# Kernel tuning notes

Measured on AMD Instinct MI355X. Metric: run time of the kernel, lower is better.

## Reference

```python
import jax, jax.numpy as jnp
import numpy as np

N = 32768   # nodes
E = 32768   # edges
ND, ED, GD = 12, 5, 11
H = 64
T = 4
STEPS = 3


def setup_inputs() -> dict:
    key = jax.random.key(0)
    ks = jax.random.split(key, 24)
    s = 0.05
    p = lambda k, sh: (jax.random.normal(k, sh) * s).astype(jnp.float32)
    return dict(
        x=jax.random.normal(ks[0], (N, ND), jnp.float32),
        edge_index=jax.random.randint(ks[1], (2, E), 0, N, jnp.int64),
        edge_attr=jax.random.uniform(ks[2], (E, ED), jnp.float32),
        u=jax.random.normal(ks[3], (1, GD), jnp.float32),
        Wp=p(ks[4], (H, ND + GD)), bp=p(ks[5], (H,)),
        We1=p(ks[6], (H, ED)), be1=p(ks[7], (H,)),
        We2=p(ks[8], (H * H, H)), be2=p(ks[9], (H * H,)),
        root=p(ks[10], (H, H)), conv_b=p(ks[11], (H,)),
        Wih=p(ks[12], (3 * H, H)), bih=p(ks[13], (3 * H,)),
        Whh=p(ks[14], (3 * H, H)), bhh=p(ks[15], (3 * H,)),
        Wd1=p(ks[16], (H, 2 * H + ED)), bd1=p(ks[17], (H,)),
        Wd2=p(ks[18], (H // 2, H)), bd2=p(ks[19], (H // 2,)),
        Wd3=p(ks[20], (T, H // 2)), bd3=p(ks[21], (T,)),
    )


def _forward(x, edge_index, edge_attr, u,
             Wp, bp, We1, be1, We2, be2, root, conv_b,
             Wih, bih, Whh, bhh, Wd1, bd1, Wd2, bd2, Wd3, bd3):
    n = x.shape[0]
    e = edge_attr.shape[0]
    src, dst = edge_index[0], edge_index[1]

    # input projection with broadcast global features (batch=None path)
    u_node = jnp.broadcast_to(u, (n, u.shape[-1]))
    h = jnp.tanh(jnp.concatenate([x, u_node], axis=-1) @ Wp.T + bp)

    # edge MLP -> per-edge (H,H) weight matrices; edge_attr is loop-invariant
    ew = jax.nn.relu(edge_attr @ We1.T + be1) @ We2.T + be2   # (E, H*H)
    ew = ew.reshape(e, H, H)                                   # (E, H, H)

    # mean-aggregation denominators (clamped to 1 like scatter-mean)
    counts = jnp.clip(jax.ops.segment_sum(jnp.ones((e,), h.dtype), dst, num_segments=n), 1.0)

    for _ in range(STEPS):
        # NNConv: gather src features, per-edge matmul, scatter-mean into dst
        msg = jnp.einsum('eh,eho->eo', h[src], ew)             # (E, H)
        agg = jax.ops.segment_sum(msg, dst, num_segments=n) / counts[:, None]
        m = jax.nn.relu(agg + h @ root + conv_b)               # dropout off (eval)
        # GRUCell (torch gate order: r, z, n)
        gi = m @ Wih.T + bih
        gh = h @ Whh.T + bhh
        r = jax.nn.sigmoid(gi[:, :H] + gh[:, :H])
        z = jax.nn.sigmoid(gi[:, H:2 * H] + gh[:, H:2 * H])
        ng = jnp.tanh(gi[:, 2 * H:] + r * gh[:, 2 * H:])
        h = (1.0 - z) * ng + z * h

    # per-edge decoder
    e_in = jnp.concatenate([h[src], h[dst], edge_attr], axis=-1)
    d = jax.nn.relu(e_in @ Wd1.T + bd1)
    d = jax.nn.relu(d @ Wd2.T + bd2)
    return d @ Wd3.T + bd3                                     # (E, T)


def reference(x, edge_index, edge_attr, u,
              Wp, bp, We1, be1, We2, be2, root, conv_b,
              Wih, bih, Whh, bhh, Wd1, bd1, Wd2, bd2, Wd3, bd3):
    return _forward(x, edge_index, edge_attr, u,
                    Wp, bp, We1, be1, We2, be2, root, conv_b,
                    Wih, bih, Whh, bhh, Wd1, bd1, Wd2, bd2, Wd3, bd3)
```

## Files before the change

### kernel.cpp

```cpp
#include <hip/hip_runtime.h>
#include <hip/hip_bf16.h>
#include <stdint.h>


#define N_NODES 32768
#define N_EDGES 32768
#define STEPS 3

typedef __attribute__((ext_vector_type(8))) short short8;
typedef __attribute__((ext_vector_type(4))) float float4v;

__device__ __forceinline__ float bf2f(unsigned short u) {
    union { unsigned int i; float f; } v; v.i = ((unsigned int)u) << 16; return v.f;
}
__device__ __forceinline__ unsigned short f2bf(float f) {
    union { float f; unsigned int i; } v; v.f = f;
    unsigned int x = v.i;
    return (unsigned short)((x + 0x7fffu + ((x >> 16) & 1u)) >> 16);
}
__device__ __forceinline__ unsigned int fbits(float f) {
    union { float f; unsigned int i; } v; v.f = f; return v.i;
}

__device__ __forceinline__ short8 packA(float hv, const float* hf) {
    union { short8 v; unsigned int u[4]; } r;
#pragma unroll
    for (int p = 0; p < 4; p++) {
        unsigned int p0 = fbits(hv * hf[2 * p]) + 0x8000u;
        unsigned int p1 = fbits(hv * hf[2 * p + 1]) + 0x8000u;
        r.u[p] = __builtin_amdgcn_perm(p1, p0, 0x07060302u);
    }
    return r.v;
}

__device__ __forceinline__ void gload_lds16(const void* g, void* l) {
    __builtin_amdgcn_global_load_lds(
        (__attribute__((address_space(1))) void*)g,
        (__attribute__((address_space(3))) void*)l, 16, 0, 0);
}

__global__ __launch_bounds__(256) void k_setup(
    const float* __restrict__ root, const float* __restrict__ Wih,
    const float* __restrict__ Whh,
    const float* __restrict__ We2, const float* __restrict__ be2,
    const float* __restrict__ Wd1, const float* __restrict__ bd1,
    const float* __restrict__ Wd2,
    const float* __restrict__ x, const float* __restrict__ u,
    const float* __restrict__ Wp, const float* __restrict__ bp,
    const float* __restrict__ ea, const float* __restrict__ We1,
    const float* __restrict__ be1,
    unsigned short* __restrict__ rootTf, unsigned short* __restrict__ wcombf,
    unsigned short* __restrict__ w2tf,
    unsigned short* __restrict__ wd1f, unsigned short* __restrict__ wd2f,
    unsigned short* __restrict__ hb,
    unsigned short* __restrict__ hid, float* __restrict__ aggcnt)
{
    int b = blockIdx.x, tid = threadIdx.x;
    if (b < 144) {
        int i = b * 256 + tid;
        if (i < 4096) {
            int j = i & 7, lane = (i >> 3) & 63, g = i >> 9;
            int kb = g >> 2, nf = g & 3;
            int o = nf * 16 + (lane & 15);
            int k = kb * 32 + (lane >> 4) * 8 + j;
            rootTf[i] = f2bf(root[k * 64 + o]);
        } else if (i < 4096 + 32768) {
            int t = i - 4096;
            int j = t & 7, lane = (t >> 3) & 63, g = t >> 9;
            int kb = g >> 4, nf = g & 15;
            int cp = nf * 16 + (lane & 15);
            int k = kb * 32 + (lane >> 4) * 8 + j;
            float v;
            if (cp < 128)      v = (k < 64) ? Wih[cp * 64 + k] : Whh[cp * 64 + (k - 64)];
            else if (cp < 192) v = (k < 64) ? Wih[cp * 64 + k] : 0.f;
            else               v = (k < 64) ? 0.f : Whh[(cp - 64) * 64 + (k - 64)];
            wcombf[t] = f2bf(v);
        }
    } else if (b < 1184) {
        int t = (b - 144) * 256 + tid;
        if (t < 65 * 4096) {
            int kk = t >> 12, r = t & 4095;
            int j = r & 7, lane = (r >> 3) & 63, g = r >> 9;
            int half = g >> 2, nf = g & 3;
            int o = nf * 16 + (lane & 15);
            int hh = half * 32 + (lane >> 4) * 8 + j;
            float v = (kk < 64) ? We2[((size_t)(hh * 64 + o)) * 64 + kk]
                                : be2[(size_t)hh * 64 + o];
            w2tf[t] = f2bf(v);
        }
    } else if (b < 1232) {
        int i = (b - 1184) * 256 + tid;
        if (i < 10240) {
            int j = i & 7, lane = (i >> 3) & 63, g = i >> 9;
            int kb = g >> 2, nf = g & 3;
            int o = nf * 16 + (lane & 15);
            int k = kb * 32 + (lane >> 4) * 8 + j;
            float v = (k < 133) ? Wd1[(size_t)o * 133 + k] : (k == 133 ? bd1[o] : 0.f);
            wd1f[i] = f2bf(v);
        } else if (i < 10240 + 2048) {
            int t = i - 10240;
            int j = t & 7, lane = (t >> 3) & 63, g = t >> 9;
            int kb = g >> 1, nf = g & 1;
            int o = nf * 16 + (lane & 15);
            int k = kb * 32 + (lane >> 4) * 8 + j;
            wd2f[t] = f2bf(Wd2[(size_t)o * 64 + k]);
        }
    } else if (b < 9424) {
        int idx = (b - 1232) * 256 + tid;
        int n = idx >> 6, j = idx & 63;
        const float* wr = Wp + j * 23;
        const float* xr = x + (size_t)n * 12;
        float s = bp[j];
#pragma unroll
        for (int i = 0; i < 12; i++) s += xr[i] * wr[i];
#pragma unroll
        for (int i = 0; i < 11; i++) s += u[i] * wr[12 + i];
        hb[idx] = f2bf(tanhf(s));
    } else if (b < 17616) {
        int idx = (b - 9424) * 256 + tid;
        int e = idx >> 6, j = idx & 63;
        float s = be1[j];
#pragma unroll
        for (int i = 0; i < 5; i++) s += ea[(size_t)e * 5 + i] * We1[j * 5 + i];
        hid[idx] = f2bf(s > 0.f ? s : 0.f);
    } else {
        int idx = (b - 17616) * 1024 + tid * 4;
        if (idx < 2129920) {
            float4v z = {0.f, 0.f, 0.f, 0.f};
            *(float4v*)(aggcnt + idx) = z;
        }
    }
}

__global__ __launch_bounds__(256) void k_counts(
    const int* __restrict__ ei, float* __restrict__ counts)
{
    int i = blockIdx.x * 256 + threadIdx.x;
    if (i < N_EDGES) atomicAdd(&counts[ei[N_EDGES + i]], 1.0f);
}

__global__ __launch_bounds__(512, 4) void k_msg_fused(
    const unsigned short* __restrict__ hid,
    const unsigned short* __restrict__ hb,
    const unsigned short* __restrict__ w2tf,
    const int* __restrict__ ei,
    float* __restrict__ agg)
{
    __shared__ unsigned short buf[2][2][8192];
    int tid = threadIdx.x, wave = tid >> 6, lane = tid & 63;
    int l15 = lane & 15, quad = lane >> 4;
    int mf = wave & 3, kh = wave >> 2;
    int ebase = blockIdx.x * 64 + mf * 16;
    int e_a = ebase + l15;
    int src = ei[e_a];

    union { short8 v[4]; unsigned short u[32]; } hrow;
#pragma unroll
    for (int i = 0; i < 4; i++)
        hrow.v[i] = *(const short8*)(hid + (size_t)e_a * 64 + kh * 32 + i * 8);

    float hf0[8], hf1[8];
    {
        short8 h0 = *(const short8*)(hb + (size_t)src * 64 + quad * 8);
        short8 h1 = *(const short8*)(hb + (size_t)src * 64 + 32 + quad * 8);
#pragma unroll
        for (int j = 0; j < 8; j++) {
            hf0[j] = bf2f((unsigned short)h0[j]);
            hf1[j] = bf2f((unsigned short)h1[j]);
        }
    }

    int kk0 = kh ? 32 : 0;
    auto stage = [&](int pair, int db) {
        const unsigned short* g = w2tf + (size_t)(kk0 + 2 * pair) * 4096;
#pragma unroll
        for (int c = 0; c < 4; c++) {
            int chunk = mf * 4 + c;
            gload_lds16(g + (size_t)chunk * 512 + lane * 8, &buf[kh][db][chunk * 512]);
        }
    };

    stage(0, 0);

    float4v acc[4] = {};
    int cur = 0;
#pragma unroll
    for (int i = 0; i <= 16; i++) {
        __syncthreads();
        if ((kh == 0 && i + 1 < 16) || (kh == 1 && i + 1 <= 16))
            stage(i + 1, cur ^ 1);
        int nkk = (kh == 0) ? (i < 16 ? 2 : 0) : (i < 16 ? 2 : 1);
        for (int s = 0; s < nkk; s++) {
            float hv = (kh == 1 && i == 16) ? 1.0f : bf2f(hrow.u[2 * i + s]);
            short8 a0 = packA(hv, hf0);
            short8 a1 = packA(hv, hf1);
            const unsigned short* bp = &buf[kh][cur][s * 4096];
#pragma unroll
            for (int nf = 0; nf < 4; nf++) {
                short8 b0 = *(const short8*)(bp + (0 * 4 + nf) * 512 + lane * 8);
                acc[nf] = __builtin_amdgcn_mfma_f32_16x16x32_bf16(a0, b0, acc[nf], 0, 0, 0);
            }
#pragma unroll
            for (int nf = 0; nf < 4; nf++) {
                short8 b1 = *(const short8*)(bp + (1 * 4 + nf) * 512 + lane * 8);
                acc[nf] = __builtin_amdgcn_mfma_f32_16x16x32_bf16(a1, b1, acc[nf], 0, 0, 0);
            }
        }
        cur ^= 1;
    }

    __syncthreads();
    float* mg = (float*)&buf[0][0][0];
    if (kh == 1) {
#pragma unroll
        for (int nf = 0; nf < 4; nf++)
#pragma unroll
            for (int r = 0; r < 4; r++)
                mg[mf * 1024 + lane * 16 + nf * 4 + r] = acc[nf][r];
    }
    __syncthreads();
    if (kh == 0) {
        int dsts[4];
#pragma unroll
        for (int r = 0; r < 4; r++) dsts[r] = ei[N_EDGES + ebase + quad * 4 + r];
#pragma unroll
        for (int nf = 0; nf < 4; nf++)
#pragma unroll
            for (int r = 0; r < 4; r++)
                atomicAdd(agg + (size_t)dsts[r] * 64 + nf * 16 + l15,
                          acc[nf][r] + mg[mf * 1024 + lane * 16 + nf * 4 + r]);
    }
}

__global__ __launch_bounds__(256) void k_node(
    const unsigned short* __restrict__ hb_in,
    const unsigned short* __restrict__ rootTf,
    const unsigned short* __restrict__ wcombf,
    float* __restrict__ agg, const float* __restrict__ counts,
    const float* __restrict__ conv_b,
    const float* __restrict__ bih, const float* __restrict__ bhh,
    unsigned short* __restrict__ hb_out)
{
    __shared__ unsigned short m_lds[64 * 72];
    int tid = threadIdx.x, w = tid >> 6, lane = tid & 63;
    int l15 = lane & 15, quad = lane >> 4;
    int node0 = blockIdx.x * 64;
    int row0 = w * 16;

    float4v acc1[4] = {};
    {
        short8 a1[2];
#pragma unroll
        for (int kb = 0; kb < 2; kb++)
            a1[kb] = *(const short8*)(hb_in + (size_t)(node0 + row0 + l15) * 64 + kb * 32 + quad * 8);
#pragma unroll
        for (int kb = 0; kb < 2; kb++)
#pragma unroll
            for (int nf = 0; nf < 4; nf++) {
                short8 b = *(const short8*)(rootTf + (size_t)((kb * 4 + nf) * 64 + lane) * 8);
                acc1[nf] = __builtin_amdgcn_mfma_f32_16x16x32_bf16(a1[kb], b, acc1[nf], 0, 0, 0);
            }
    }
#pragma unroll
    for (int rr = 0; rr < 4; rr++) {
        int nl = row0 + quad * 4 + rr;
        float cnt = counts[node0 + nl]; if (cnt < 1.f) cnt = 1.f;
        float rcp = 1.f / cnt;
#pragma unroll
        for (int nf = 0; nf < 4; nf++) {
            int c = nf * 16 + l15;
            float* ap = agg + (size_t)(node0 + nl) * 64 + c;
            float av = *ap;
            *ap = 0.f;
            float mv = av * rcp + acc1[nf][rr] + conv_b[c];
            m_lds[nl * 72 + c] = f2bf(mv > 0.f ? mv : 0.f);
        }
    }
    __syncthreads();

    float4v acc2[16] = {};
#pragma unroll
    for (int kb = 0; kb < 4; kb++) {
        short8 a2;
        if (kb < 2)
            a2 = *(const short8*)(m_lds + (row0 + l15) * 72 + kb * 32 + quad * 8);
        else
            a2 = *(const short8*)(hb_in + (size_t)(node0 + row0 + l15) * 64 + (kb - 2) * 32 + quad * 8);
#pragma unroll
        for (int nf = 0; nf < 16; nf++) {
            short8 b = *(const short8*)(wcombf + (size_t)((kb * 16 + nf) * 64 + lane) * 8);
            acc2[nf] = __builtin_amdgcn_mfma_f32_16x16x32_bf16(a2, b, acc2[nf], 0, 0, 0);
        }
    }

#pragma unroll
    for (int nf0 = 0; nf0 < 4; nf0++) {
        int c = nf0 * 16 + l15;
        float br = bih[c] + bhh[c];
        float bz = bih[64 + c] + bhh[64 + c];
        float bni = bih[128 + c], bnh = bhh[128 + c];
#pragma unroll
        for (int rr = 0; rr < 4; rr++) {
            int node = node0 + row0 + quad * 4 + rr;
            float gr = 1.f / (1.f + __expf(-(acc2[nf0][rr] + br)));
            float gz = 1.f / (1.f + __expf(-(acc2[nf0 + 4][rr] + bz)));
            float ng = tanhf(acc2[nf0 + 8][rr] + bni + gr * (acc2[nf0 + 12][rr] + bnh));
            float ho = bf2f(hb_in[(size_t)node * 64 + c]);
            float hn = (1.f - gz) * ng + gz * ho;
            hb_out[(size_t)node * 64 + c] = f2bf(hn);
        }
    }
}

__global__ __launch_bounds__(256) void k_decoder(
    const unsigned short* __restrict__ hb, const int* __restrict__ ei,
    const float* __restrict__ ea,
    const unsigned short* __restrict__ wd1f, const unsigned short* __restrict__ wd2f,
    const float* __restrict__ bd2,
    const float* __restrict__ Wd3, const float* __restrict__ bd3,
    float* __restrict__ out)
{
    __shared__ unsigned short d1f[4][1024];
    __shared__ float d2s[4][16 * 33];
    int tid = threadIdx.x, w = tid >> 6, lane = tid & 63;
    int l15 = lane & 15, quad = lane >> 4;
    int ebase = blockIdx.x * 64 + w * 16;
    int e = ebase + l15;
    int src = ei[e], dst = ei[N_EDGES + e];

    short8 a[5];
#pragma unroll
    for (int kb = 0; kb < 2; kb++) {
        a[kb]     = *(const short8*)(hb + (size_t)src * 64 + kb * 32 + quad * 8);
        a[2 + kb] = *(const short8*)(hb + (size_t)dst * 64 + kb * 32 + quad * 8);
    }
    {
        union { short8 v; unsigned short u[8]; } tea;
#pragma unroll
        for (int j = 0; j < 8; j++) {
            float vv = 0.f;
            if (quad == 0) vv = (j < 5) ? ea[(size_t)e * 5 + j] : (j == 5 ? 1.f : 0.f);
            tea.u[j] = f2bf(vv);
        }
        a[4] = tea.v;
    }

    float4v acc1[4] = {};
#pragma unroll
    for (int kb = 0; kb < 5; kb++)
#pragma unroll
        for (int nf = 0; nf < 4; nf++) {
            short8 b = *(const short8*)(wd1f + (size_t)((kb * 4 + nf) * 64 + lane) * 8);
            acc1[nf] = __builtin_amdgcn_mfma_f32_16x16x32_bf16(a[kb], b, acc1[nf], 0, 0, 0);
        }
#pragma unroll
    for (int nf = 0; nf < 4; nf++) {
        int kbp = nf >> 1;
        int lanep_hi = ((nf & 1) * 2 + (l15 >> 3)) * 16;
        int jp = l15 & 7;
#pragma unroll
        for (int r = 0; r < 4; r++) {
            float v = acc1[nf][r];
            d1f[w][kbp * 512 + (lanep_hi + quad * 4 + r) * 8 + jp] = f2bf(v > 0.f ? v : 0.f);
        }
    }
    float4v acc2[2] = {};
#pragma unroll
    for (int kb = 0; kb < 2; kb++) {
        short8 a2 = *(const short8*)(&d1f[w][kb * 512 + lane * 8]);
#pragma unroll
        for (int nf = 0; nf < 2; nf++) {
            short8 b = *(const short8*)(wd2f + (size_t)((kb * 2 + nf) * 64 + lane) * 8);
            acc2[nf] = __builtin_amdgcn_mfma_f32_16x16x32_bf16(a2, b, acc2[nf], 0, 0, 0);
        }
    }
#pragma unroll
    for (int nf = 0; nf < 2; nf++) {
        int c = nf * 16 + l15;
        float bias = bd2[c];
#pragma unroll
        for (int r = 0; r < 4; r++) {
            float v = acc2[nf][r] + bias;
            d2s[w][(quad * 4 + r) * 33 + c] = v > 0.f ? v : 0.f;
        }
    }
    {
        int e_l = lane >> 2, t = lane & 3;
        float s = bd3[t];
        const float* w3 = Wd3 + t * 32;
        const float* dr = &d2s[w][e_l * 33];
#pragma unroll
        for (int k = 0; k < 32; k++) s += w3[k] * dr[k];
        out[(size_t)(ebase + e_l) * 4 + t] = s;
    }
}

extern "C" void kernel_launch(void* const* d_in, const int* in_sizes, int n_in,
                              void* d_out, int out_size, void* d_ws, size_t ws_size,
                              hipStream_t stream)
{
    const float* x      = (const float*)d_in[0];
    const int*   ei     = (const int*)d_in[1];
    const float* ea     = (const float*)d_in[2];
    const float* u      = (const float*)d_in[3];
    const float* Wp     = (const float*)d_in[4];
    const float* bp     = (const float*)d_in[5];
    const float* We1    = (const float*)d_in[6];
    const float* be1    = (const float*)d_in[7];
    const float* We2    = (const float*)d_in[8];
    const float* be2    = (const float*)d_in[9];
    const float* root   = (const float*)d_in[10];
    const float* conv_b = (const float*)d_in[11];
    const float* Wih    = (const float*)d_in[12];
    const float* bih    = (const float*)d_in[13];
    const float* Whh    = (const float*)d_in[14];
    const float* bhh    = (const float*)d_in[15];
    const float* Wd1    = (const float*)d_in[16];
    const float* bd1    = (const float*)d_in[17];
    const float* Wd2    = (const float*)d_in[18];
    const float* bd2    = (const float*)d_in[19];
    const float* Wd3    = (const float*)d_in[20];
    const float* bd3    = (const float*)d_in[21];
    float* out = (float*)d_out;

    char* ws = (char*)d_ws;
    size_t off = 0;
    auto take = [&](size_t bytes) -> char* {
        char* p = ws + off; off = (off + bytes + 255) & ~(size_t)255; return p;
    };
    unsigned short* hb     = (unsigned short*)take((size_t)N_NODES * 64 * 2);
    unsigned short* hid    = (unsigned short*)take((size_t)N_EDGES * 64 * 2);
    float*          aggcnt = (float*)take((size_t)(N_NODES * 64 + N_NODES) * 4);
    float*          agg    = aggcnt;
    float*          cnts   = aggcnt + (size_t)N_NODES * 64;
    unsigned short* w2tf   = (unsigned short*)take((size_t)66 * 4096 * 2);
    unsigned short* rootTf = (unsigned short*)take((size_t)4096 * 2);
    unsigned short* wcombf = (unsigned short*)take((size_t)32768 * 2);
    unsigned short* wd1f   = (unsigned short*)take((size_t)10240 * 2);
    unsigned short* wd2f   = (unsigned short*)take((size_t)2048 * 2);
    (void)ws_size;

    k_setup<<<19696, 256, 0, stream>>>(root, Wih, Whh, We2, be2, Wd1, bd1, Wd2,
                                       x, u, Wp, bp, ea, We1, be1,
                                       rootTf, wcombf, w2tf, wd1f, wd2f,
                                       hb, hid, aggcnt);
    k_counts<<<128, 256, 0, stream>>>(ei, cnts);

    for (int s = 0; s < STEPS; s++) {
        k_msg_fused<<<N_EDGES / 64, 512, 0, stream>>>(hid, hb, w2tf, ei, agg);
        k_node<<<N_NODES / 64, 256, 0, stream>>>(hb, rootTf, wcombf, agg, cnts,
                                                 conv_b, bih, bhh, hb);
    }
    k_decoder<<<N_EDGES / 64, 256, 0, stream>>>(hb, ei, ea, wd1f, wd2f, bd2,
                                                Wd3, bd3, out);
}
```

Before: 267.0 us.

## Switch bf16 storage and MFMA to fp16 with packed half2 products

Converts all stored activations and weights from bf16 to fp16 and uses f16 MFMA instructions throughout. In the message kernel the per-edge A operand is now built with packed half2 multiplies instead of fp32 multiplies followed by manual bf16 rounding and perm packing, which cuts VALU work in the hot loop. It also removes the full unroll of the main k-loop and pads the LDS reduction buffer stride to 17 to avoid bank conflicts. Using fp16 narrows dynamic range, which could matter for the edge-weight products, and dropping the unroll may add loop overhead.

```diff
diff --git a/kernel.cpp b/kernel.cpp
--- a/kernel.cpp
+++ b/kernel.cpp
@@ -8,28 +8,21 @@
 #define STEPS 3
 
 typedef __attribute__((ext_vector_type(8))) short short8;
+typedef __attribute__((ext_vector_type(8))) _Float16 half8;
+typedef __attribute__((ext_vector_type(2))) _Float16 half2v;
 typedef __attribute__((ext_vector_type(4))) float float4v;
 
-__device__ __forceinline__ float bf2f(unsigned short u) {
-    union { unsigned int i; float f; } v; v.i = ((unsigned int)u) << 16; return v.f;
-}
-__device__ __forceinline__ unsigned short f2bf(float f) {
-    union { float f; unsigned int i; } v; v.f = f;
-    unsigned int x = v.i;
-    return (unsigned short)((x + 0x7fffu + ((x >> 16) & 1u)) >> 16);
-}
-__device__ __forceinline__ unsigned int fbits(float f) {
-    union { float f; unsigned int i; } v; v.f = f; return v.i;
-}
-
-__device__ __forceinline__ short8 packA(float hv, const float* hf) {
-    union { short8 v; unsigned int u[4]; } r;
-#pragma unroll
-    for (int p = 0; p < 4; p++) {
-        unsigned int p0 = fbits(hv * hf[2 * p]) + 0x8000u;
-        unsigned int p1 = fbits(hv * hf[2 * p + 1]) + 0x8000u;
-        r.u[p] = __builtin_amdgcn_perm(p1, p0, 0x07060302u);
-    }
+__device__ __forceinline__ unsigned short f2h(float f) {
+    union { _Float16 h; unsigned short u; } c; c.h = (_Float16)f; return c.u;
+}
+__device__ __forceinline__ float h2f(unsigned short u) {
+    union { unsigned short u; _Float16 h; } c; c.u = u; return (float)c.h;
+}
+
+__device__ __forceinline__ half8 packA(half2v hv2, const half2v* hp) {
+    union { half8 v; half2v h[4]; } r;
+#pragma unroll
+    for (int p = 0; p < 4; p++) r.h[p] = hv2 * hp[p];
     return r.v;
 }
 
@@ -63,7 +56,7 @@
             int kb = g >> 2, nf = g & 3;
             int o = nf * 16 + (lane & 15);
             int k = kb * 32 + (lane >> 4) * 8 + j;
-            rootTf[i] = f2bf(root[k * 64 + o]);
+            rootTf[i] = f2h(root[k * 64 + o]);
         } else if (i < 4096 + 32768) {
             int t = i - 4096;
             int j = t & 7, lane = (t >> 3) & 63, g = t >> 9;
@@ -74,7 +67,7 @@
             if (cp < 128)      v = (k < 64) ? Wih[cp * 64 + k] : Whh[cp * 64 + (k - 64)];
             else if (cp < 192) v = (k < 64) ? Wih[cp * 64 + k] : 0.f;
             else               v = (k < 64) ? 0.f : Whh[(cp - 64) * 64 + (k - 64)];
-            wcombf[t] = f2bf(v);
+            wcombf[t] = f2h(v);
         }
     } else if (b < 1184) {
         int t = (b - 144) * 256 + tid;
@@ -86,7 +79,7 @@
             int hh = half * 32 + (lane >> 4) * 8 + j;
             float v = (kk < 64) ? We2[((size_t)(hh * 64 + o)) * 64 + kk]
                                 : be2[(size_t)hh * 64 + o];
-            w2tf[t] = f2bf(v);
+            w2tf[t] = f2h(v);
         }
     } else if (b < 1232) {
         int i = (b - 1184) * 256 + tid;
@@ -96,14 +89,14 @@
             int o = nf * 16 + (lane & 15);
             int k = kb * 32 + (lane >> 4) * 8 + j;
             float v = (k < 133) ? Wd1[(size_t)o * 133 + k] : (k == 133 ? bd1[o] : 0.f);
-            wd1f[i] = f2bf(v);
+            wd1f[i] = f2h(v);
         } else if (i < 10240 + 2048) {
             int t = i - 10240;
             int j = t & 7, lane = (t >> 3) & 63, g = t >> 9;
             int kb = g >> 1, nf = g & 1;
             int o = nf * 16 + (lane & 15);
             int k = kb * 32 + (lane >> 4) * 8 + j;
-            wd2f[t] = f2bf(Wd2[(size_t)o * 64 + k]);
+            wd2f[t] = f2h(Wd2[(size_t)o * 64 + k]);
         }
     } else if (b < 9424) {
         int idx = (b - 1232) * 256 + tid;
@@ -115,14 +108,14 @@
         for (int i = 0; i < 12; i++) s += xr[i] * wr[i];
 #pragma unroll
         for (int i = 0; i < 11; i++) s += u[i] * wr[12 + i];
-        hb[idx] = f2bf(tanhf(s));
+        hb[idx] = f2h(tanhf(s));
     } else if (b < 17616) {
         int idx = (b - 9424) * 256 + tid;
         int e = idx >> 6, j = idx & 63;
         float s = be1[j];
 #pragma unroll
         for (int i = 0; i < 5; i++) s += ea[(size_t)e * 5 + i] * We1[j * 5 + i];
-        hid[idx] = f2bf(s > 0.f ? s : 0.f);
+        hid[idx] = f2h(s > 0.f ? s : 0.f);
     } else {
         int idx = (b - 17616) * 1024 + tid * 4;
         if (idx < 2129920) {
@@ -159,16 +152,9 @@
     for (int i = 0; i < 4; i++)
         hrow.v[i] = *(const short8*)(hid + (size_t)e_a * 64 + kh * 32 + i * 8);
 
-    float hf0[8], hf1[8];
-    {
-        short8 h0 = *(const short8*)(hb + (size_t)src * 64 + quad * 8);
-        short8 h1 = *(const short8*)(hb + (size_t)src * 64 + 32 + quad * 8);
-#pragma unroll
-        for (int j = 0; j < 8; j++) {
-            hf0[j] = bf2f((unsigned short)h0[j]);
-            hf1[j] = bf2f((unsigned short)h1[j]);
-        }
-    }
+    union Hp { half8 v; half2v p[4]; } hf0, hf1;
+    hf0.v = *(const half8*)(hb + (size_t)src * 64 + quad * 8);
+    hf1.v = *(const half8*)(hb + (size_t)src * 64 + 32 + quad * 8);
 
     int kk0 = kh ? 32 : 0;
     auto stage = [&](int pair, int db) {
@@ -179,31 +165,32 @@
             gload_lds16(g + (size_t)chunk * 512 + lane * 8, &buf[kh][db][chunk * 512]);
         }
     };
-
     stage(0, 0);
 
     float4v acc[4] = {};
     int cur = 0;
-#pragma unroll
     for (int i = 0; i <= 16; i++) {
         __syncthreads();
         if ((kh == 0 && i + 1 < 16) || (kh == 1 && i + 1 <= 16))
             stage(i + 1, cur ^ 1);
         int nkk = (kh == 0) ? (i < 16 ? 2 : 0) : (i < 16 ? 2 : 1);
         for (int s = 0; s < nkk; s++) {
-            float hv = (kh == 1 && i == 16) ? 1.0f : bf2f(hrow.u[2 * i + s]);
-            short8 a0 = packA(hv, hf0);
-            short8 a1 = packA(hv, hf1);
             const unsigned short* bp = &buf[kh][cur][s * 4096];
+            unsigned short hu = (kh == 1 && i == 16) ? (unsigned short)0x3C00
+                                                     : hrow.u[(2 * i + s) & 31];
+            union { unsigned short u; _Float16 h; } cv; cv.u = hu;
+            half2v hv2 = { cv.h, cv.h };
+            half8 a0 = packA(hv2, hf0.p);
+            half8 a1 = packA(hv2, hf1.p);
 #pragma unroll
             for (int nf = 0; nf < 4; nf++) {
-                short8 b0 = *(const short8*)(bp + (0 * 4 + nf) * 512 + lane * 8);
-                acc[nf] = __builtin_amdgcn_mfma_f32_16x16x32_bf16(a0, b0, acc[nf], 0, 0, 0);
+                half8 b0 = *(const half8*)(bp + (0 * 4 + nf) * 512 + lane * 8);
+                acc[nf] = __builtin_amdgcn_mfma_f32_16x16x32_f16(a0, b0, acc[nf], 0, 0, 0);
             }
 #pragma unroll
             for (int nf = 0; nf < 4; nf++) {
-                short8 b1 = *(const short8*)(bp + (1 * 4 + nf) * 512 + lane * 8);
-                acc[nf] = __builtin_amdgcn_mfma_f32_16x16x32_bf16(a1, b1, acc[nf], 0, 0, 0);
+                half8 b1 = *(const half8*)(bp + (1 * 4 + nf) * 512 + lane * 8);
+                acc[nf] = __builtin_amdgcn_mfma_f32_16x16x32_f16(a1, b1, acc[nf], 0, 0, 0);
             }
         }
         cur ^= 1;
@@ -216,7 +203,7 @@
         for (int nf = 0; nf < 4; nf++)
 #pragma unroll
             for (int r = 0; r < 4; r++)
-                mg[mf * 1024 + lane * 16 + nf * 4 + r] = acc[nf][r];
+                mg[(mf * 64 + lane) * 17 + nf * 4 + r] = acc[nf][r];
     }
     __syncthreads();
     if (kh == 0) {
@@ -228,7 +215,7 @@
 #pragma unroll
             for (int r = 0; r < 4; r++)
                 atomicAdd(agg + (size_t)dsts[r] * 64 + nf * 16 + l15,
-                          acc[nf][r] + mg[mf * 1024 + lane * 16 + nf * 4 + r]);
+                          acc[nf][r] + mg[(mf * 64 + lane) * 17 + nf * 4 + r]);
     }
 }
 
@@ -249,16 +236,16 @@
 
     float4v acc1[4] = {};
     {
-        short8 a1[2];
+        half8 a1[2];
 #pragma unroll
         for (int kb = 0; kb < 2; kb++)
-            a1[kb] = *(const short8*)(hb_in + (size_t)(node0 + row0 + l15) * 64 + kb * 32 + quad * 8);
+            a1[kb] = *(const half8*)(hb_in + (size_t)(node0 + row0 + l15) * 64 + kb * 32 + quad * 8);
 #pragma unroll
         for (int kb = 0; kb < 2; kb++)
 #pragma unroll
             for (int nf = 0; nf < 4; nf++) {
-                short8 b = *(const short8*)(rootTf + (size_t)((kb * 4 + nf) * 64 + lane) * 8);
-                acc1[nf] = __builtin_amdgcn_mfma_f32_16x16x32_bf16(a1[kb], b, acc1[nf], 0, 0, 0);
+                half8 b = *(const half8*)(rootTf + (size_t)((kb * 4 + nf) * 64 + lane) * 8);
+                acc1[nf] = __builtin_amdgcn_mfma_f32_16x16x32_f16(a1[kb], b, acc1[nf], 0, 0, 0);
             }
     }
 #pragma unroll
@@ -273,7 +260,7 @@
             float av = *ap;
             *ap = 0.f;
             float mv = av * rcp + acc1[nf][rr] + conv_b[c];
-            m_lds[nl * 72 + c] = f2bf(mv > 0.f ? mv : 0.f);
+            m_lds[nl * 72 + c] = f2h(mv > 0.f ? mv : 0.f);
         }
     }
     __syncthreads();
@@ -281,15 +268,15 @@
     float4v acc2[16] = {};
 #pragma unroll
     for (int kb = 0; kb < 4; kb++) {
-        short8 a2;
+        half8 a2;
         if (kb < 2)
-            a2 = *(const short8*)(m_lds + (row0 + l15) * 72 + kb * 32 + quad * 8);
+            a2 = *(const half8*)(m_lds + (row0 + l15) * 72 + kb * 32 + quad * 8);
         else
-            a2 = *(const short8*)(hb_in + (size_t)(node0 + row0 + l15) * 64 + (kb - 2) * 32 + quad * 8);
+            a2 = *(const half8*)(hb_in + (size_t)(node0 + row0 + l15) * 64 + (kb - 2) * 32 + quad * 8);
 #pragma unroll
         for (int nf = 0; nf < 16; nf++) {
-            short8 b = *(const short8*)(wcombf + (size_t)((kb * 16 + nf) * 64 + lane) * 8);
-            acc2[nf] = __builtin_amdgcn_mfma_f32_16x16x32_bf16(a2, b, acc2[nf], 0, 0, 0);
+            half8 b = *(const half8*)(wcombf + (size_t)((kb * 16 + nf) * 64 + lane) * 8);
+            acc2[nf] = __builtin_amdgcn_mfma_f32_16x16x32_f16(a2, b, acc2[nf], 0, 0, 0);
         }
     }
 
@@ -305,9 +292,9 @@
             float gr = 1.f / (1.f + __expf(-(acc2[nf0][rr] + br)));
             float gz = 1.f / (1.f + __expf(-(acc2[nf0 + 4][rr] + bz)));
             float ng = tanhf(acc2[nf0 + 8][rr] + bni + gr * (acc2[nf0 + 12][rr] + bnh));
-            float ho = bf2f(hb_in[(size_t)node * 64 + c]);
+            float ho = h2f(hb_in[(size_t)node * 64 + c]);
             float hn = (1.f - gz) * ng + gz * ho;
-            hb_out[(size_t)node * 64 + c] = f2bf(hn);
+            hb_out[(size_t)node * 64 + c] = f2h(hn);
         }
     }
 }
@@ -328,19 +315,19 @@
     int e = ebase + l15;
     int src = ei[e], dst = ei[N_EDGES + e];
 
-    short8 a[5];
+    half8 a[5];
 #pragma unroll
     for (int kb = 0; kb < 2; kb++) {
-        a[kb]     = *(const short8*)(hb + (size_t)src * 64 + kb * 32 + quad * 8);
-        a[2 + kb] = *(const short8*)(hb + (size_t)dst * 64 + kb * 32 + quad * 8);
+        a[kb]     = *(const half8*)(hb + (size_t)src * 64 + kb * 32 + quad * 8);
+        a[2 + kb] = *(const half8*)(hb + (size_t)dst * 64 + kb * 32 + quad * 8);
     }
     {
-        union { short8 v; unsigned short u[8]; } tea;
+        union { half8 v; unsigned short u[8]; } tea;
 #pragma unroll
         for (int j = 0; j < 8; j++) {
             float vv = 0.f;
             if (quad == 0) vv = (j < 5) ? ea[(size_t)e * 5 + j] : (j == 5 ? 1.f : 0.f);
-            tea.u[j] = f2bf(vv);
+            tea.u[j] = f2h(vv);
         }
         a[4] = tea.v;
     }
@@ -350,8 +337,8 @@
     for (int kb = 0; kb < 5; kb++)
 #pragma unroll
         for (int nf = 0; nf < 4; nf++) {
-            short8 b = *(const short8*)(wd1f + (size_t)((kb * 4 + nf) * 64 + lane) * 8);
-            acc1[nf] = __builtin_amdgcn_mfma_f32_16x16x32_bf16(a[kb], b, acc1[nf], 0, 0, 0);
+            half8 b = *(const half8*)(wd1f + (size_t)((kb * 4 + nf) * 64 + lane) * 8);
+            acc1[nf] = __builtin_amdgcn_mfma_f32_16x16x32_f16(a[kb], b, acc1[nf], 0, 0, 0);
         }
 #pragma unroll
     for (int nf = 0; nf < 4; nf++) {
@@ -361,17 +348,17 @@
 #pragma unroll
         for (int r = 0; r < 4; r++) {
             float v = acc1[nf][r];
-            d1f[w][kbp * 512 + (lanep_hi + quad * 4 + r) * 8 + jp] = f2bf(v > 0.f ? v : 0.f);
+            d1f[w][kbp * 512 + (lanep_hi + quad * 4 + r) * 8 + jp] = f2h(v > 0.f ? v : 0.f);
         }
     }
     float4v acc2[2] = {};
 #pragma unroll
     for (int kb = 0; kb < 2; kb++) {
-        short8 a2 = *(const short8*)(&d1f[w][kb * 512 + lane * 8]);
+        half8 a2 = *(const half8*)(&d1f[w][kb * 512 + lane * 8]);
 #pragma unroll
         for (int nf = 0; nf < 2; nf++) {
-            short8 b = *(const short8*)(wd2f + (size_t)((kb * 2 + nf) * 64 + lane) * 8);
-            acc2[nf] = __builtin_amdgcn_mfma_f32_16x16x32_bf16(a2, b, acc2[nf], 0, 0, 0);
+            half8 b = *(const half8*)(wd2f + (size_t)((kb * 2 + nf) * 64 + lane) * 8);
+            acc2[nf] = __builtin_amdgcn_mfma_f32_16x16x32_f16(a2, b, acc2[nf], 0, 0, 0);
         }
     }
 #pragma unroll
```

After: 303.7 us. +13.7%, slower.
